# Performance work log

Measured on AMD Instinct MI355X. Metric: run time of the kernel, lower is better.

## Reference

```python
import jax, jax.numpy as jnp
import numpy as np


def setup_inputs() -> dict:
    key = jax.random.key(0)
    ks = jax.random.split(key, 5)
    B, T, C = 4, 2048, 2048
    n_heads = 16
    sc = 0.02
    return {
        "x": jax.random.normal(ks[0], (B, T, C), dtype=jnp.float32),
        "Wqkv": jax.random.normal(ks[1], (3 * C, C), dtype=jnp.float32) * sc,
        "bqkv": jax.random.normal(ks[2], (3 * C,), dtype=jnp.float32) * sc,
        "Wout": jax.random.normal(ks[3], (C, C), dtype=jnp.float32) * sc,
        "bout": jax.random.normal(ks[4], (C,), dtype=jnp.float32) * sc,
        "n_heads": n_heads,
    }


def reference(x, Wqkv, bqkv, Wout, bout, n_heads):
    B, T, C = x.shape
    hd = C // n_heads
    qkv = x @ Wqkv.T + bqkv                      # [B, T, 3C]
    q, k, v = jnp.split(qkv, 3, axis=-1)
    # [B, T, C] -> [B, nH, T, hd]
    def heads(t):
        return t.reshape(B, T, n_heads, hd).transpose(0, 2, 1, 3)
    q, k, v = heads(q), heads(k), heads(v)
    new_k, new_v = k, v
    att = jnp.einsum('bhqd,bhkd->bhqk', q, k) / jnp.sqrt(jnp.float32(hd))
    T_total = k.shape[2]
    # torch.tril(ones(T, T_total)): allow j <= i (standard causal when T_total == T)
    mask = jnp.tril(jnp.ones((T, T_total), dtype=bool))
    att = jnp.where(mask, att, -jnp.inf)
    att = jax.nn.softmax(att, axis=-1)
    y = jnp.einsum('bhqk,bhkd->bhqd', att, v)    # [B, nH, T, hd]
    y = y.transpose(0, 2, 1, 3).reshape(B, T, C)
    y = y @ Wout.T + bout
    return (y, new_k, new_v)
```

## Files before the change

### kernel.cpp

```cpp
#include <hip/hip_runtime.h>
#include <hip/hip_bf16.h>

typedef __attribute__((ext_vector_type(8))) short bf16x8;
typedef __attribute__((ext_vector_type(4))) float f32x4;

__device__ __forceinline__ unsigned short f2bf(float f) {
  unsigned u = __float_as_uint(f);
  u += 0x7fffu + ((u >> 16) & 1u);
  return (unsigned short)(u >> 16);
}

__device__ __forceinline__ void gload16(const void* g, void* l) {
  __builtin_amdgcn_global_load_lds(
      (const __attribute__((address_space(1))) void*)g,
      (__attribute__((address_space(3))) void*)l, 16, 0, 0);
}

__global__ void cvt_bf16(const float* __restrict__ in, unsigned short* __restrict__ out, int n4) {
  int i = blockIdx.x * blockDim.x + threadIdx.x;
  int st = gridDim.x * blockDim.x;
  for (; i < n4; i += st) {
    float4 f = ((const float4*)in)[i];
    ushort4 o;
    o.x = f2bf(f.x); o.y = f2bf(f.y); o.z = f2bf(f.z); o.w = f2bf(f.w);
    ((ushort4*)out)[i] = o;
  }
}

template<int EPI>
__global__ __launch_bounds__(256) void gemm_bt(
    const unsigned short* __restrict__ A,
    const unsigned short* __restrict__ B,
    const float* __restrict__ bias,
    float* __restrict__ outF,
    unsigned short* __restrict__ q_ws,
    unsigned short* __restrict__ k_ws,
    unsigned short* __restrict__ v_wst,
    float* __restrict__ out_k,
    float* __restrict__ out_v,
    int M, int N, int K)
{
  __shared__ __align__(16) unsigned short As[2][128 * 64];
  __shared__ __align__(16) unsigned short Bs[2][128 * 64];

  const int nbx = N >> 7;
  int nwg = gridDim.x;
  int bid = blockIdx.x;
  int cpx = nwg >> 3;
  int sw  = (bid & 7) * cpx + (bid >> 3);
  int bx = sw % nbx, by = sw / nbx;
  const int m0 = by << 7, n0 = bx << 7;

  const int tid = threadIdx.x, w = tid >> 6, ln = tid & 63;
  const int wm = w >> 1, wn = w & 1;
  const int srow = ln >> 3;
  const int scol = (ln & 7) * 8;
  const int lg = ln >> 4, lc = ln & 15;

  f32x4 acc[4][4] = {};

  auto STAGE = [&](int bf, int k0) {
#pragma unroll
    for (int i = 0; i < 4; ++i) {
      int row = w * 32 + i * 8 + srow;
      gload16(A + (size_t)(m0 + row) * K + k0 + scol, &As[bf][(w * 32 + i * 8) * 64]);
      gload16(B + (size_t)(n0 + row) * K + k0 + scol, &Bs[bf][(w * 32 + i * 8) * 64]);
    }
  };

  const int nt = K >> 6;
  STAGE(0, 0);
  for (int t = 0; t < nt; ++t) {
    __syncthreads();
    if (t + 1 < nt) STAGE((t + 1) & 1, (t + 1) << 6);
    const unsigned short* as = As[t & 1];
    const unsigned short* bs = Bs[t & 1];
#pragma unroll
    for (int kk = 0; kk < 2; ++kk) {
      bf16x8 af[4], bfr[4];
      int ko = kk * 32 + lg * 8;
#pragma unroll
      for (int m = 0; m < 4; ++m) af[m]  = *(const bf16x8*)&as[(wm * 64 + m * 16 + lc) * 64 + ko];
#pragma unroll
      for (int n = 0; n < 4; ++n) bfr[n] = *(const bf16x8*)&bs[(wn * 64 + n * 16 + lc) * 64 + ko];
#pragma unroll
      for (int m = 0; m < 4; ++m)
#pragma unroll
        for (int n = 0; n < 4; ++n)
          acc[m][n] = __builtin_amdgcn_mfma_f32_16x16x32_bf16(af[m], bfr[n], acc[m][n], 0, 0, 0);
    }
  }

  const int lr = lg * 4;
  if (EPI == 0) {
#pragma unroll
    for (int m = 0; m < 4; ++m) {
      int r0 = m0 + wm * 64 + m * 16 + lr;
#pragma unroll
      for (int n = 0; n < 4; ++n) {
        int c = n0 + wn * 64 + n * 16 + lc;
        float bv = bias[c];
#pragma unroll
        for (int r = 0; r < 4; ++r)
          outF[(size_t)(r0 + r) * N + c] = acc[m][n][r] + bv;
      }
    }
  } else {
    const int sel = n0 >> 11;
    const int h   = (n0 >> 7) & 15;
    const int b   = m0 >> 11;
    const size_t hb = (size_t)(b * 16 + h);
#pragma unroll
    for (int m = 0; m < 4; ++m) {
      int t0 = (m0 & 2047) + wm * 64 + m * 16 + lr;
#pragma unroll
      for (int n = 0; n < 4; ++n) {
        int d = wn * 64 + n * 16 + lc;
        float bv = bias[n0 + d];
        float v0 = acc[m][n][0] + bv, v1 = acc[m][n][1] + bv;
        float v2 = acc[m][n][2] + bv, v3 = acc[m][n][3] + bv;
        size_t base = (hb * 2048 + t0) * 128 + d;
        if (sel == 0) {
          q_ws[base      ] = f2bf(v0);
          q_ws[base + 128] = f2bf(v1);
          q_ws[base + 256] = f2bf(v2);
          q_ws[base + 384] = f2bf(v3);
        } else if (sel == 1) {
          out_k[base] = v0; out_k[base + 128] = v1; out_k[base + 256] = v2; out_k[base + 384] = v3;
          k_ws[base      ] = f2bf(v0);
          k_ws[base + 128] = f2bf(v1);
          k_ws[base + 256] = f2bf(v2);
          k_ws[base + 384] = f2bf(v3);
        } else {
          out_v[base] = v0; out_v[base + 128] = v1; out_v[base + 256] = v2; out_v[base + 384] = v3;
          ushort4 pk; pk.x = f2bf(v0); pk.y = f2bf(v1); pk.z = f2bf(v2); pk.w = f2bf(v3);
          *(ushort4*)&v_wst[(hb * 128 + d) * 2048 + t0] = pk;
        }
      }
    }
  }
}

__global__ __launch_bounds__(256) void attn_fwd(
    const unsigned short* __restrict__ q_ws,
    const unsigned short* __restrict__ k_ws,
    const unsigned short* __restrict__ v_wst,
    unsigned short* __restrict__ y_ws)
{
  __shared__ __align__(16) unsigned short K_lds[2][64 * 128];
  __shared__ __align__(16) unsigned short Vt_lds[2][128 * 64];
  __shared__ __align__(16) unsigned short P_lds[128 * 64];

  int bid = blockIdx.x;
  int sw = (bid & 7) * 128 + (bid >> 3);
  const int bh = sw >> 4;
  const int qb = sw & 15;
  const int q0 = qb << 7;
  const int tid = threadIdx.x, w = tid >> 6, ln = tid & 63;
  const int lg = ln >> 4, lc = ln & 15;
  const int b = bh >> 4, h = bh & 15;

  bf16x8 qf[2][4];
  {
    const unsigned short* qp = q_ws + ((size_t)bh * 2048 + q0 + w * 32) * 128;
#pragma unroll
    for (int m = 0; m < 2; ++m)
#pragma unroll
      for (int ks = 0; ks < 4; ++ks)
        qf[m][ks] = *(const bf16x8*)&qp[(m * 16 + lc) * 128 + ks * 32 + lg * 8];
  }

  float lsum[2] = {0.f, 0.f};
  f32x4 o[2][8] = {};

  auto STAGE = [&](int bf, int kv0) {
#pragma unroll
    for (int i = 0; i < 4; ++i) {
      int rowK = w * 16 + i * 4 + lg;
      int gK = (lc * 16) ^ ((rowK & 7) << 4);
      gload16(k_ws + ((size_t)bh * 2048 + kv0 + rowK) * 128 + (gK >> 1),
              &K_lds[bf][(w * 16 + i * 4) * 128]);
      int rowV = w * 32 + i * 8 + (ln >> 3);
      int gV = ((ln & 7) * 16) ^ ((rowV & 7) << 4);
      gload16(v_wst + ((size_t)bh * 128 + rowV) * 2048 + kv0 + (gV >> 1),
              &Vt_lds[bf][(w * 32 + i * 8) * 64]);
    }
  };

  const int ntiles = (q0 >> 6) + 2;
  STAGE(0, 0);
  const float scl = 0.08838834764831845f;

  for (int t = 0; t < ntiles; ++t) {
    const int kv0 = t << 6;
    __syncthreads();
    if (t + 1 < ntiles) STAGE((t + 1) & 1, (t + 1) << 6);
    if (kv0 > q0 + w * 32 + 31) continue;
    const unsigned short* Kl = K_lds[t & 1];
    const unsigned short* Vl = Vt_lds[t & 1];

    f32x4 s[2][4] = {};
#pragma unroll
    for (int ks = 0; ks < 4; ++ks) {
      bf16x8 kb[4];
#pragma unroll
      for (int n = 0; n < 4; ++n) {
        int row = n * 16 + lc;
        int cb = (ks * 64 + lg * 16) ^ ((row & 7) << 4);
        kb[n] = *(const bf16x8*)((const char*)Kl + row * 256 + cb);
      }
#pragma unroll
      for (int m = 0; m < 2; ++m)
#pragma unroll
        for (int n = 0; n < 4; ++n)
          s[m][n] = __builtin_amdgcn_mfma_f32_16x16x32_bf16(kb[n], qf[m][ks], s[m][n], 0, 0, 0);
    }

#pragma unroll
    for (int m = 0; m < 2; ++m) {
      const int rowg = q0 + w * 32 + m * 16 + lc;
      const int prow = w * 32 + m * 16 + lc;
      const unsigned swz = (unsigned)((prow & 7) << 4);
#pragma unroll
      for (int n = 0; n < 4; ++n) {
        const int colg = kv0 + n * 16 + lg * 4;
        float p0 = (colg + 0 > rowg) ? 0.f : __expf(s[m][n][0] * scl);
        float p1 = (colg + 1 > rowg) ? 0.f : __expf(s[m][n][1] * scl);
        float p2 = (colg + 2 > rowg) ? 0.f : __expf(s[m][n][2] * scl);
        float p3 = (colg + 3 > rowg) ? 0.f : __expf(s[m][n][3] * scl);
        lsum[m] += (p0 + p1) + (p2 + p3);
        ushort4 pk;
        pk.x = f2bf(p0); pk.y = f2bf(p1); pk.z = f2bf(p2); pk.w = f2bf(p3);
        *(ushort4*)((char*)P_lds + prow * 128 + ((unsigned)(n * 32 + lg * 8) ^ swz)) = pk;
      }
    }

#pragma unroll
    for (int ks = 0; ks < 2; ++ks) {
      bf16x8 pbf[2], vb[8];
#pragma unroll
      for (int m = 0; m < 2; ++m) {
        int prow = w * 32 + m * 16 + lc;
        int cb = (ks * 64 + lg * 16) ^ ((prow & 7) << 4);
        pbf[m] = *(const bf16x8*)((const char*)P_lds + prow * 128 + cb);
      }
#pragma unroll
      for (int n8 = 0; n8 < 8; ++n8) {
        int row = n8 * 16 + lc;
        int cb = (ks * 64 + lg * 16) ^ ((row & 7) << 4);
        vb[n8] = *(const bf16x8*)((const char*)Vl + row * 128 + cb);
      }
#pragma unroll
      for (int m = 0; m < 2; ++m)
#pragma unroll
        for (int n8 = 0; n8 < 8; ++n8)
          o[m][n8] = __builtin_amdgcn_mfma_f32_16x16x32_bf16(vb[n8], pbf[m], o[m][n8], 0, 0, 0);
    }
  }

  float inv[2];
#pragma unroll
  for (int m = 0; m < 2; ++m) {
    float ls = lsum[m];
    ls += __shfl_xor(ls, 16);
    ls += __shfl_xor(ls, 32);
    inv[m] = 1.f / ls;
  }
  const size_t bb = (size_t)b * 2048;
#pragma unroll
  for (int m = 0; m < 2; ++m) {
    int rowg = q0 + w * 32 + m * 16 + lc;
    unsigned short* yp = y_ws + (bb + rowg) * 2048 + h * 128;
#pragma unroll
    for (int n8 = 0; n8 < 8; ++n8) {
      ushort4 pk;
      pk.x = f2bf(o[m][n8][0] * inv[m]);
      pk.y = f2bf(o[m][n8][1] * inv[m]);
      pk.z = f2bf(o[m][n8][2] * inv[m]);
      pk.w = f2bf(o[m][n8][3] * inv[m]);
      *(ushort4*)&yp[n8 * 16 + lg * 4] = pk;
    }
  }
}

extern "C" void kernel_launch(void* const* d_in, const int* in_sizes, int n_in,
                              void* d_out, int out_size, void* d_ws, size_t ws_size,
                              hipStream_t stream) {
  const float* x    = (const float*)d_in[0];
  const float* Wqkv = (const float*)d_in[1];
  const float* bqkv = (const float*)d_in[2];
  const float* Wout = (const float*)d_in[3];
  const float* bout = (const float*)d_in[4];

  float* y_out = (float*)d_out;
  float* k_out = y_out + (size_t)16777216;
  float* v_out = y_out + (size_t)33554432;

  unsigned short* xb    = (unsigned short*)d_ws;
  unsigned short* wqkvb = xb + 16777216;
  unsigned short* woutb = wqkvb + 12582912;
  unsigned short* q_ws  = woutb + 4194304;
  unsigned short* k_ws  = q_ws + 16777216;
  unsigned short* v_wst = k_ws + 16777216;
  unsigned short* y_ws  = v_wst + 16777216;

  cvt_bf16<<<2048, 256, 0, stream>>>(x, xb, 16777216 / 4);
  cvt_bf16<<<2048, 256, 0, stream>>>(Wqkv, wqkvb, 12582912 / 4);
  cvt_bf16<<<1024, 256, 0, stream>>>(Wout, woutb, 4194304 / 4);

  gemm_bt<1><<<3072, 256, 0, stream>>>(xb, wqkvb, bqkv, nullptr,
                                       q_ws, k_ws, v_wst, k_out, v_out,
                                       8192, 6144, 2048);

  attn_fwd<<<1024, 256, 0, stream>>>(q_ws, k_ws, v_wst, y_ws);

  gemm_bt<0><<<1024, 256, 0, stream>>>(y_ws, woutb, bout, y_out,
                                       nullptr, nullptr, nullptr, nullptr, nullptr,
                                       8192, 2048, 2048);
}
```

Before: 845.4 us.

## Enlarge GEMM tiles to 256x256 with 8 waves, swizzled LDS and explicit waitcnt pipeline

Both GEMMs move from 128x128 tiles with 4 waves to 256x256 tiles with 8 waves per workgroup, so each wave accumulates a 128x64 sub-tile. The LDS layout is XOR-swizzled to avoid bank conflicts on fragment reads. The main loop replaces __syncthreads with explicit vmcnt waits and raw barriers, interleaves fragment loads with MFMA groups under raised priority, and the QKV epilogue now computes the head index per column. Larger tiles raise arithmetic intensity but increase register and LDS pressure and shrink the grid, which may leave CUs underused for the output GEMM, which now has only 256 workgroups.

```diff
diff --git a/kernel.cpp b/kernel.cpp
--- a/kernel.cpp
+++ b/kernel.cpp
@@ -28,7 +28,7 @@
 }
 
 template<int EPI>
-__global__ __launch_bounds__(256) void gemm_bt(
+__global__ __launch_bounds__(512, 2) void gemm_bt(
     const unsigned short* __restrict__ A,
     const unsigned short* __restrict__ B,
     const float* __restrict__ bias,
@@ -40,85 +40,154 @@
     float* __restrict__ out_v,
     int M, int N, int K)
 {
-  __shared__ __align__(16) unsigned short As[2][128 * 64];
-  __shared__ __align__(16) unsigned short Bs[2][128 * 64];
-
-  const int nbx = N >> 7;
+  __shared__ __align__(16) unsigned short As[2][16384];
+  __shared__ __align__(16) unsigned short Bs[2][16384];
+
+  const int nbx = N >> 8;
   int nwg = gridDim.x;
   int bid = blockIdx.x;
   int cpx = nwg >> 3;
   int sw  = (bid & 7) * cpx + (bid >> 3);
   int bx = sw % nbx, by = sw / nbx;
-  const int m0 = by << 7, n0 = bx << 7;
+  const int m0 = by << 8, n0 = bx << 8;
 
   const int tid = threadIdx.x, w = tid >> 6, ln = tid & 63;
-  const int wm = w >> 1, wn = w & 1;
-  const int srow = ln >> 3;
-  const int scol = (ln & 7) * 8;
+  const int wm = w >> 2, wn = w & 3;
   const int lg = ln >> 4, lc = ln & 15;
 
-  f32x4 acc[4][4] = {};
+  const int srow = tid >> 3;
+  const int scol = ((ln & 7) ^ (srow & 7)) * 8;
+
+  f32x4 acc[8][4] = {};
 
   auto STAGE = [&](int bf, int k0) {
 #pragma unroll
-    for (int i = 0; i < 4; ++i) {
-      int row = w * 32 + i * 8 + srow;
-      gload16(A + (size_t)(m0 + row) * K + k0 + scol, &As[bf][(w * 32 + i * 8) * 64]);
-      gload16(B + (size_t)(n0 + row) * K + k0 + scol, &Bs[bf][(w * 32 + i * 8) * 64]);
-    }
+    for (int i = 0; i < 4; ++i)
+      gload16(A + (size_t)(m0 + i * 64 + srow) * K + k0 + scol,
+              &As[bf][i * 4096 + w * 512]);
+#pragma unroll
+    for (int i = 0; i < 4; ++i)
+      gload16(B + (size_t)(n0 + i * 64 + srow) * K + k0 + scol,
+              &Bs[bf][i * 4096 + w * 512]);
+  };
+
+  auto rdA = [&](const unsigned short* as, int mh, int mf, int ks) -> bf16x8 {
+    int r = wm * 128 + mh * 64 + mf * 16 + lc;
+    int cb = (ks * 64 + lg * 16) ^ ((r & 7) << 4);
+    return *(const bf16x8*)((const char*)as + r * 128 + cb);
+  };
+  auto rdB = [&](const unsigned short* bs, int nh, int nf, int ks) -> bf16x8 {
+    int r = wn * 64 + (nh * 2 + nf) * 16 + lc;
+    int cb = (ks * 64 + lg * 16) ^ ((r & 7) << 4);
+    return *(const bf16x8*)((const char*)bs + r * 128 + cb);
   };
 
   const int nt = K >> 6;
   STAGE(0, 0);
   for (int t = 0; t < nt; ++t) {
-    __syncthreads();
-    if (t + 1 < nt) STAGE((t + 1) & 1, (t + 1) << 6);
     const unsigned short* as = As[t & 1];
     const unsigned short* bs = Bs[t & 1];
-#pragma unroll
-    for (int kk = 0; kk < 2; ++kk) {
-      bf16x8 af[4], bfr[4];
-      int ko = kk * 32 + lg * 8;
-#pragma unroll
-      for (int m = 0; m < 4; ++m) af[m]  = *(const bf16x8*)&as[(wm * 64 + m * 16 + lc) * 64 + ko];
-#pragma unroll
-      for (int n = 0; n < 4; ++n) bfr[n] = *(const bf16x8*)&bs[(wn * 64 + n * 16 + lc) * 64 + ko];
-#pragma unroll
-      for (int m = 0; m < 4; ++m)
-#pragma unroll
-        for (int n = 0; n < 4; ++n)
-          acc[m][n] = __builtin_amdgcn_mfma_f32_16x16x32_bf16(af[m], bfr[n], acc[m][n], 0, 0, 0);
-    }
-  }
-
-  const int lr = lg * 4;
+    if (t + 1 < nt) {
+      STAGE((t + 1) & 1, (t + 1) << 6);
+      asm volatile("s_waitcnt vmcnt(8)" ::: "memory");
+    } else {
+      asm volatile("s_waitcnt vmcnt(0)" ::: "memory");
+    }
+    __builtin_amdgcn_sched_barrier(0);
+    asm volatile("s_barrier" ::: "memory");
+    __builtin_amdgcn_sched_barrier(0);
+
+    bf16x8 a[4][2], b[2][2];
+#pragma unroll
+    for (int mf = 0; mf < 4; ++mf)
+#pragma unroll
+      for (int ks = 0; ks < 2; ++ks) a[mf][ks] = rdA(as, 0, mf, ks);
+#pragma unroll
+    for (int nf = 0; nf < 2; ++nf)
+#pragma unroll
+      for (int ks = 0; ks < 2; ++ks) b[nf][ks] = rdB(bs, 0, nf, ks);
+    __builtin_amdgcn_s_setprio(1);
+#pragma unroll
+    for (int ks = 0; ks < 2; ++ks)
+#pragma unroll
+      for (int mf = 0; mf < 4; ++mf)
+#pragma unroll
+        for (int nf = 0; nf < 2; ++nf)
+          acc[mf][nf] = __builtin_amdgcn_mfma_f32_16x16x32_bf16(a[mf][ks], b[nf][ks], acc[mf][nf], 0, 0, 0);
+    __builtin_amdgcn_s_setprio(0);
+#pragma unroll
+    for (int nf = 0; nf < 2; ++nf)
+#pragma unroll
+      for (int ks = 0; ks < 2; ++ks) b[nf][ks] = rdB(bs, 1, nf, ks);
+    __builtin_amdgcn_s_setprio(1);
+#pragma unroll
+    for (int ks = 0; ks < 2; ++ks)
+#pragma unroll
+      for (int mf = 0; mf < 4; ++mf)
+#pragma unroll
+        for (int nf = 0; nf < 2; ++nf)
+          acc[mf][2 + nf] = __builtin_amdgcn_mfma_f32_16x16x32_bf16(a[mf][ks], b[nf][ks], acc[mf][2 + nf], 0, 0, 0);
+    __builtin_amdgcn_s_setprio(0);
+#pragma unroll
+    for (int mf = 0; mf < 4; ++mf)
+#pragma unroll
+      for (int ks = 0; ks < 2; ++ks) a[mf][ks] = rdA(as, 1, mf, ks);
+    __builtin_amdgcn_s_setprio(1);
+#pragma unroll
+    for (int ks = 0; ks < 2; ++ks)
+#pragma unroll
+      for (int mf = 0; mf < 4; ++mf)
+#pragma unroll
+        for (int nf = 0; nf < 2; ++nf)
+          acc[4 + mf][2 + nf] = __builtin_amdgcn_mfma_f32_16x16x32_bf16(a[mf][ks], b[nf][ks], acc[4 + mf][2 + nf], 0, 0, 0);
+    __builtin_amdgcn_s_setprio(0);
+#pragma unroll
+    for (int nf = 0; nf < 2; ++nf)
+#pragma unroll
+      for (int ks = 0; ks < 2; ++ks) b[nf][ks] = rdB(bs, 0, nf, ks);
+    __builtin_amdgcn_s_setprio(1);
+#pragma unroll
+    for (int ks = 0; ks < 2; ++ks)
+#pragma unroll
+      for (int mf = 0; mf < 4; ++mf)
+#pragma unroll
+        for (int nf = 0; nf < 2; ++nf)
+          acc[4 + mf][nf] = __builtin_amdgcn_mfma_f32_16x16x32_bf16(a[mf][ks], b[nf][ks], acc[4 + mf][nf], 0, 0, 0);
+    __builtin_amdgcn_s_setprio(0);
+
+    __builtin_amdgcn_sched_barrier(0);
+    asm volatile("s_barrier" ::: "memory");
+    __builtin_amdgcn_sched_barrier(0);
+  }
+
   if (EPI == 0) {
 #pragma unroll
-    for (int m = 0; m < 4; ++m) {
-      int r0 = m0 + wm * 64 + m * 16 + lr;
-#pragma unroll
-      for (int n = 0; n < 4; ++n) {
-        int c = n0 + wn * 64 + n * 16 + lc;
+    for (int m8 = 0; m8 < 8; ++m8) {
+      int r0 = m0 + wm * 128 + m8 * 16 + lg * 4;
+#pragma unroll
+      for (int n4 = 0; n4 < 4; ++n4) {
+        int c = n0 + wn * 64 + n4 * 16 + lc;
         float bv = bias[c];
 #pragma unroll
         for (int r = 0; r < 4; ++r)
-          outF[(size_t)(r0 + r) * N + c] = acc[m][n][r] + bv;
+          outF[(size_t)(r0 + r) * N + c] = acc[m8][n4][r] + bv;
       }
     }
   } else {
     const int sel = n0 >> 11;
-    const int h   = (n0 >> 7) & 15;
-    const int b   = m0 >> 11;
-    const size_t hb = (size_t)(b * 16 + h);
-#pragma unroll
-    for (int m = 0; m < 4; ++m) {
-      int t0 = (m0 & 2047) + wm * 64 + m * 16 + lr;
-#pragma unroll
-      for (int n = 0; n < 4; ++n) {
-        int d = wn * 64 + n * 16 + lc;
-        float bv = bias[n0 + d];
-        float v0 = acc[m][n][0] + bv, v1 = acc[m][n][1] + bv;
-        float v2 = acc[m][n][2] + bv, v3 = acc[m][n][3] + bv;
+    const int b_  = m0 >> 11;
+#pragma unroll
+    for (int m8 = 0; m8 < 8; ++m8) {
+      int t0 = (m0 & 2047) + wm * 128 + m8 * 16 + lg * 4;
+#pragma unroll
+      for (int n4 = 0; n4 < 4; ++n4) {
+        int dg = n0 + wn * 64 + n4 * 16 + lc;
+        int h  = (dg >> 7) & 15;
+        int d  = dg & 127;
+        const size_t hb = (size_t)(b_ * 16 + h);
+        float bv = bias[dg];
+        float v0 = acc[m8][n4][0] + bv, v1 = acc[m8][n4][1] + bv;
+        float v2 = acc[m8][n4][2] + bv, v3 = acc[m8][n4][3] + bv;
         size_t base = (hb * 2048 + t0) * 128 + d;
         if (sel == 0) {
           q_ws[base      ] = f2bf(v0);
@@ -308,13 +377,13 @@
   cvt_bf16<<<2048, 256, 0, stream>>>(Wqkv, wqkvb, 12582912 / 4);
   cvt_bf16<<<1024, 256, 0, stream>>>(Wout, woutb, 4194304 / 4);
 
-  gemm_bt<1><<<3072, 256, 0, stream>>>(xb, wqkvb, bqkv, nullptr,
-                                       q_ws, k_ws, v_wst, k_out, v_out,
-                                       8192, 6144, 2048);
+  gemm_bt<1><<<768, 512, 0, stream>>>(xb, wqkvb, bqkv, nullptr,
+                                      q_ws, k_ws, v_wst, k_out, v_out,
+                                      8192, 6144, 2048);
 
   attn_fwd<<<1024, 256, 0, stream>>>(q_ws, k_ws, v_wst, y_ws);
 
-  gemm_bt<0><<<1024, 256, 0, stream>>>(y_ws, woutb, bout, y_out,
-                                       nullptr, nullptr, nullptr, nullptr, nullptr,
-                                       8192, 2048, 2048);
-}
+  gemm_bt<0><<<256, 512, 0, stream>>>(y_ws, woutb, bout, y_out,
+                                      nullptr, nullptr, nullptr, nullptr, nullptr,
+                                      8192, 2048, 2048);
+}
```

Result: faster. 740.1 us (-12.5%).
